# Performance work log

Hardware: AMD Instinct MI355X
Metric: run time of the kernel (lower is better)

## Reference

```python
import jax, jax.numpy as jnp
import numpy as np

EMBED_DIM = 1024
HEAD_NUM = 16
NEG = 100000.0


def setup_inputs() -> dict:
    key = jax.random.key(0)
    k1, k2, k3, k4, k5 = jax.random.split(key, 5)
    B, S, E = 2, 2048, EMBED_DIM
    return {
        "x": jax.random.normal(k1, (B, S, E), dtype=jnp.float32),
        "w_attn": jax.random.normal(k2, (E, 3 * E), dtype=jnp.float32) * 0.02,
        "b_attn": jax.random.normal(k3, (3 * E,), dtype=jnp.float32) * 0.02,
        "w_proj": jax.random.normal(k4, (E, E), dtype=jnp.float32) * 0.02,
        "b_proj": jax.random.normal(k5, (E,), dtype=jnp.float32) * 0.02,
    }


def reference(x, w_attn, b_attn, w_proj, b_proj):
    B, S, E = x.shape
    H = HEAD_NUM
    d = E // H
    dk = jnp.asarray(d, x.dtype) ** 0.5  # (embed_dim // head_num) ** 0.5

    qkv = x @ w_attn + b_attn                      # [B, S, 3E]
    qkv = qkv.reshape(B, S, H, 3 * d)              # split heads BEFORE chunk (as in source)
    qkv = jnp.swapaxes(qkv, 1, 2)                  # [B, H, S, 3d]
    q, k, v = jnp.split(qkv, 3, axis=-1)           # each [B, H, S, d]

    w = jnp.einsum("bhqd,bhkd->bhqk", q, k) / dk   # [B, H, S, S]
    mask = jnp.tril(jnp.ones((S, S), dtype=x.dtype))
    w = w * mask - (1.0 - mask) * NEG              # exact masking math of source
    w = jax.nn.softmax(w, axis=-1)                 # dropout omitted (eval mode)

    a = jnp.einsum("bhqk,bhkd->bhqd", w, v)        # [B, H, S, d]
    a = jnp.swapaxes(a, 1, 2).reshape(B, S, E)     # [B, S, E]
    h = a @ w_proj + b_proj                        # resi dropout omitted (eval mode)
    return h
```

## Files before the change

### kernel.cpp

```cpp
#include <hip/hip_runtime.h>
#include <hip/hip_bf16.h>

#define BB 2
#define SS 2048
#define EE 1024
#define HH 16
#define DD 64
#define MM (BB*SS)
#define N1 (3*EE)

typedef __attribute__((ext_vector_type(4))) float f32x4;
typedef __attribute__((ext_vector_type(16))) float f32x16;
typedef __attribute__((ext_vector_type(8))) short bf16x8;
typedef __attribute__((ext_vector_type(4))) unsigned int u32x4;
typedef __attribute__((ext_vector_type(2))) unsigned int u32x2;

__device__ __forceinline__ ushort f2bf(float f){
  union { float f; unsigned u; } v; v.f = f;
  unsigned r = v.u + 0x7fffu + ((v.u >> 16) & 1u);
  return (ushort)(r >> 16);
}

__device__ __forceinline__ float bf2f(ushort u){
  union { unsigned u; float f; } v; v.u = ((unsigned)u) << 16; return v.f;
}

__device__ __forceinline__ unsigned cvt_pk(float a, float b){
  unsigned r; asm("v_cvt_pk_bf16_f32 %0, %1, %2" : "=v"(r) : "v"(a), "v"(b)); return r;
}

__device__ __forceinline__ float exp2_fast(float x){
  float r; asm("v_exp_f32 %0, %1" : "=v"(r) : "v"(x)); return r;
}

__device__ __forceinline__ u32x2 pl32swap(unsigned a, unsigned b){
  return __builtin_amdgcn_permlane32_swap(a, b, false, false);
}

__device__ __forceinline__ void gload16(const void* g, void* l){
  __builtin_amdgcn_global_load_lds(
      (const __attribute__((address_space(1))) unsigned*)g,
      (__attribute__((address_space(3))) unsigned*)l, 16, 0, 0);
}

__global__ __launch_bounds__(256) void prep_kernel(const float* __restrict__ x, ushort* __restrict__ xb,
    const float* __restrict__ wa, ushort* __restrict__ waT,
    const float* __restrict__ wp, ushort* __restrict__ wpT){
  __shared__ float t[32][33];
  const int bid = blockIdx.x, tid = threadIdx.x;
  if (bid < 4096){
    int i = bid*256 + tid;
    const float4 f = reinterpret_cast<const float4*>(x)[i];
    ushort4 o; o.x=f2bf(f.x); o.y=f2bf(f.y); o.z=f2bf(f.z); o.w=f2bf(f.w);
    reinterpret_cast<ushort4*>(xb)[i] = o;
  } else {
    const float* in; ushort* out; int N, nx, b;
    if (bid < 7168){ b = bid - 4096; in = wa; out = waT; N = N1; nx = N1/32; }
    else           { b = bid - 7168; in = wp; out = wpT; N = EE; nx = EE/32; }
    const int n0 = (b % nx)*32, k0 = (b / nx)*32;
    const int tx = tid & 31, ty = tid >> 5;
    for (int r = ty; r < 32; r += 8)
      t[r][tx] = in[(size_t)(k0+r)*N + n0 + tx];
    __syncthreads();
    for (int r = ty; r < 32; r += 8)
      out[(size_t)(n0+r)*EE + k0 + tx] = f2bf(t[tx][r]);
  }
}

__global__ __launch_bounds__(256) void gemm_qkv(const ushort* __restrict__ A,
    const ushort* __restrict__ Bt, const float* __restrict__ bias,
    ushort* __restrict__ q_, ushort* __restrict__ k_, ushort* __restrict__ v_,
    int M, int N, int K){
  __shared__ ushort As[128*64];
  __shared__ ushort Bs[128*64];
  const int tid = threadIdx.x;
  const int lane = tid & 63, w = tid >> 6;
  const int nx = gridDim.x;
  const int nwg = nx * gridDim.y;
  const int flat = blockIdx.y*nx + blockIdx.x;
  const int sw = (flat & 7)*(nwg >> 3) + (flat >> 3);
  const int m0 = (sw / nx)*128, n0 = (sw % nx)*128;
  const int wm = (w >> 1)*64, wn = (w & 1)*64;
  const int lr = lane & 15, g4 = lane >> 4;
  const int c0 = w*4;
  const int csr = lane >> 3;
  const int gcb = ((lane & 7) ^ csr)*8;
  const int sw7 = lr & 7;

  f32x4 acc[4][4] = {};
  for (int k0 = 0; k0 < K; k0 += 64){
    #pragma unroll
    for (int i = 0; i < 4; ++i){
      const int c = c0 + i;
      gload16(A  + (size_t)(m0 + c*8 + csr)*K + k0 + gcb, &As[(c*8)*64]);
      gload16(Bt + (size_t)(n0 + c*8 + csr)*K + k0 + gcb, &Bs[(c*8)*64]);
    }
    __syncthreads();
    #pragma unroll
    for (int kk = 0; kk < 2; ++kk){
      bf16x8 af[4], bfr[4];
      #pragma unroll
      for (int m = 0; m < 4; ++m)
        af[m] = *reinterpret_cast<bf16x8*>(&As[(wm + m*16 + lr)*64 + (((kk*4 + g4) ^ sw7)*8)]);
      #pragma unroll
      for (int n = 0; n < 4; ++n)
        bfr[n] = *reinterpret_cast<bf16x8*>(&Bs[(wn + n*16 + lr)*64 + (((kk*4 + g4) ^ sw7)*8)]);
      __builtin_amdgcn_s_setprio(1);
      #pragma unroll
      for (int m = 0; m < 4; ++m)
        #pragma unroll
        for (int n = 0; n < 4; ++n)
          acc[m][n] = __builtin_amdgcn_mfma_f32_16x16x32_bf16(af[m], bfr[n], acc[m][n], 0, 0, 0);
      __builtin_amdgcn_s_setprio(0);
    }
    __syncthreads();
  }
  #pragma unroll
  for (int m = 0; m < 4; ++m){
    #pragma unroll
    for (int n = 0; n < 4; ++n){
      int col = n0 + wn + n*16 + lr;
      float bv = bias[col];
      #pragma unroll
      for (int r = 0; r < 4; ++r){
        int row = m0 + wm + m*16 + (lane >> 4)*4 + r;
        float v = acc[m][n][r] + bv;
        int b = row >> 11, s = row & 2047;
        int h = col / 192, t = col - h*192;
        ushort u = f2bf(v);
        size_t bh = (size_t)(b*HH + h);
        if (t < 64)       q_[(bh*SS + s)*DD + t]        = u;
        else if (t < 128) k_[(bh*SS + s)*DD + (t-64)]   = u;
        else              v_[(bh*DD + (t-128))*SS + s]  = u;
      }
    }
  }
}

__global__ __launch_bounds__(256) void gemm_proj(const ushort* __restrict__ A,
    const ushort* __restrict__ Bt, const float* __restrict__ bias,
    float* __restrict__ of, int M, int N, int K){
  __shared__ ushort As[64*64];
  __shared__ ushort Bs[128*64];
  const int tid = threadIdx.x;
  const int lane = tid & 63, w = tid >> 6;
  const int nx = gridDim.x;
  const int nwg = nx * gridDim.y;
  const int flat = blockIdx.y*nx + blockIdx.x;
  const int sw = (flat & 7)*(nwg >> 3) + (flat >> 3);
  const int m0 = (sw / nx)*64, n0 = (sw % nx)*128;
  const int lr = lane & 15, g4 = lane >> 4;
  const int csr = lane >> 3;
  const int gcb = ((lane & 7) ^ csr)*8;
  const int sw7 = lr & 7;

  f32x4 acc[4][2] = {};
  for (int k0 = 0; k0 < K; k0 += 64){
    #pragma unroll
    for (int i = 0; i < 2; ++i){
      const int c = w*2 + i;
      gload16(A + (size_t)(m0 + c*8 + csr)*K + k0 + gcb, &As[(c*8)*64]);
    }
    #pragma unroll
    for (int i = 0; i < 4; ++i){
      const int c = w*4 + i;
      gload16(Bt + (size_t)(n0 + c*8 + csr)*K + k0 + gcb, &Bs[(c*8)*64]);
    }
    __syncthreads();
    #pragma unroll
    for (int kk = 0; kk < 2; ++kk){
      bf16x8 af[4], bfr[2];
      #pragma unroll
      for (int m = 0; m < 4; ++m)
        af[m] = *reinterpret_cast<bf16x8*>(&As[(m*16 + lr)*64 + (((kk*4 + g4) ^ sw7)*8)]);
      #pragma unroll
      for (int n = 0; n < 2; ++n)
        bfr[n] = *reinterpret_cast<bf16x8*>(&Bs[(w*32 + n*16 + lr)*64 + (((kk*4 + g4) ^ sw7)*8)]);
      __builtin_amdgcn_s_setprio(1);
      #pragma unroll
      for (int m = 0; m < 4; ++m)
        #pragma unroll
        for (int n = 0; n < 2; ++n)
          acc[m][n] = __builtin_amdgcn_mfma_f32_16x16x32_bf16(af[m], bfr[n], acc[m][n], 0, 0, 0);
      __builtin_amdgcn_s_setprio(0);
    }
    __syncthreads();
  }
  #pragma unroll
  for (int m = 0; m < 4; ++m){
    #pragma unroll
    for (int n = 0; n < 2; ++n){
      int col = n0 + w*32 + n*16 + lr;
      float bv = bias[col];
      #pragma unroll
      for (int r = 0; r < 4; ++r){
        int row = m0 + m*16 + g4*4 + r;
        of[(size_t)row*N + col] = acc[m][n][r] + bv;
      }
    }
  }
}

#define SCL 0.18033688f
__global__ __launch_bounds__(256,3) void attn2(const ushort* __restrict__ Qg,
    const ushort* __restrict__ Kg, const ushort* __restrict__ Vg,
    ushort* __restrict__ aout, ushort* __restrict__ pbuf,
    float* __restrict__ s0b, float* __restrict__ s1b){
  __shared__ __align__(16) ushort Kl[3][64*64];
  __shared__ __align__(16) ushort Vl[3][64*64];
  const int tid = threadIdx.x, lane = tid & 63, wv = tid >> 6;
  const int bh = blockIdx.x;
  const int c  = blockIdx.y;
  int qt, t0, t1, half;
  if (c < 8){ qt = c; t0 = 0; t1 = 2*(c+1); half = -1; }
  else { int i = c - 8; qt = 8 + (i >> 1); int n = qt + 1; half = i & 1;
         t0 = half ? n : 0; t1 = half ? 2*n : n; }
  const int b = bh >> 4, h = bh & 15;
  const int q0 = qt*128;
  const int ql = lane & 31, g = lane >> 5;
  const int qrow = q0 + wv*32 + ql;
  const int qminw = q0 + wv*32;
  const int qmaxw = qminw + 31;

  const ushort* Qp = Qg + ((size_t)bh*SS + qrow)*DD;
  bf16x8 qf[4];
  #pragma unroll
  for (int s = 0; s < 4; ++s)
    qf[s] = *(const bf16x8*)(Qp + s*16 + g*8);

  f32x16 ot[2] = {};
  float sr = 0.f;

  const int csr = lane >> 3;
  const int gcb = ((lane & 7) ^ csr)*8;
  const ushort* Kbase = Kg + (size_t)bh*SS*DD;
  const ushort* Vbase = Vg + (size_t)bh*DD*SS;
  const int nv = (qmaxw >> 6) + 1;
  const int swq = (ql & 7);

  auto stage = [&](int t, int bi){
    const int k0 = t*64;
    #pragma unroll
    for (int i = 0; i < 2; ++i){
      const int ch = wv*2 + i;
      gload16(Kbase + (size_t)(k0 + ch*8 + csr)*DD + gcb, &Kl[bi][(ch*8)*64]);
      gload16(Vbase + (size_t)(ch*8 + csr)*SS + k0 + gcb, &Vl[bi][(ch*8)*64]);
    }
  };

  auto qk = [&](int t, int bi, f32x16& s0, f32x16& s1){
    const ushort* Kc = &Kl[bi][0];
    f32x16 a0 = {}, a1 = {};
    __builtin_amdgcn_s_setprio(1);
    #pragma unroll
    for (int s = 0; s < 4; ++s){
      bf16x8 kf0 = *(const bf16x8*)&Kc[ ql     *64 + (((2*s + g) ^ swq)*8)];
      bf16x8 kf1 = *(const bf16x8*)&Kc[(32+ql) *64 + (((2*s + g) ^ swq)*8)];
      a0 = __builtin_amdgcn_mfma_f32_32x32x16_bf16(kf0, qf[s], a0, 0, 0, 0);
      a1 = __builtin_amdgcn_mfma_f32_32x32x16_bf16(kf1, qf[s], a1, 0, 0, 0);
    }
    __builtin_amdgcn_s_setprio(0);
    const int k0 = t*64;
    if (k0 + 63 > qminw){
      #pragma unroll
      for (int r = 0; r < 16; ++r){
        int kg0 = k0 + (r & 3) + 8*(r >> 2) + 4*g;
        a0[r] = (kg0 > qrow) ? -1e30f : a0[r];
        a1[r] = (kg0 + 32 > qrow) ? -1e30f : a1[r];
      }
    }
    s0 = a0; s1 = a1;
  };

  auto smpv = [&](int bi, f32x16& s0, f32x16& s1){
    float p[2][16];
    #pragma unroll
    for (int r = 0; r < 16; ++r){
      p[0][r] = exp2_fast(s0[r]*SCL);
      p[1][r] = exp2_fast(s1[r]*SCL);
    }
    float s8[8];
    #pragma unroll
    for (int i = 0; i < 8; ++i)
      s8[i] = (p[0][i] + p[0][i+8]) + (p[1][i] + p[1][i+8]);
    float ts = ((s8[0]+s8[1]) + (s8[2]+s8[3])) + ((s8[4]+s8[5]) + (s8[6]+s8[7]));
    { u32x2 rs = pl32swap(__float_as_uint(ts), __float_as_uint(ts));
      ts = __uint_as_float(rs[0]) + __uint_as_float(rs[1]); }
    sr += ts;

    const ushort* Vc = &Vl[bi][0];
    __builtin_amdgcn_s_setprio(1);
    #pragma unroll
    for (int kf = 0; kf < 2; ++kf){
      #pragma unroll
      for (int s2 = 0; s2 < 2; ++s2){
        const int base = s2*8;
        unsigned u0 = cvt_pk(p[kf][base+0], p[kf][base+1]);
        unsigned u1 = cvt_pk(p[kf][base+2], p[kf][base+3]);
        unsigned u2 = cvt_pk(p[kf][base+4], p[kf][base+5]);
        unsigned u3 = cvt_pk(p[kf][base+6], p[kf][base+7]);
        u32x2 r0 = pl32swap(u0, u2);
        u32x2 r1 = pl32swap(u1, u3);
        union { u32x4 u; bf16x8 hv; } pw;
        pw.u[0] = r0[0]; pw.u[1] = r1[0]; pw.u[2] = r0[1]; pw.u[3] = r1[1];
        const int cbv = 4*kf + 2*s2 + g;
        bf16x8 v0f = *(const bf16x8*)&Vc[ ql     *64 + ((cbv ^ swq)*8)];
        bf16x8 v1f = *(const bf16x8*)&Vc[(32+ql) *64 + ((cbv ^ swq)*8)];
        ot[0] = __builtin_amdgcn_mfma_f32_32x32x16_bf16(v0f, pw.hv, ot[0], 0, 0, 0);
        ot[1] = __builtin_amdgcn_mfma_f32_32x32x16_bf16(v1f, pw.hv, ot[1], 0, 0, 0);
      }
    }
    __builtin_amdgcn_s_setprio(0);
  };

  stage(t0, 0);
  stage(t0 + 1, 1);
  int bi = 0;
  for (int t = t0; t < t1; ++t){
    if (t + 1 < t1) { asm volatile("s_waitcnt vmcnt(4)" ::: "memory"); }
    else            { asm volatile("s_waitcnt vmcnt(0)" ::: "memory"); }
    __builtin_amdgcn_s_barrier();
    __builtin_amdgcn_sched_barrier(0);
    if (t + 2 < t1){
      int bs = bi + 2; if (bs >= 3) bs -= 3;
      stage(t + 2, bs);
    }
    if (t < nv){
      f32x16 s0, s1;
      qk(t, bi, s0, s1);
      smpv(bi, s0, s1);
    }
    ++bi; if (bi == 3) bi = 0;
  }

  const float inv = 1.f / sr;
  if (half == 1){
    const int pr = ((qt - 8)*32 + bh)*128 + wv*32 + ql;
    #pragma unroll
    for (int df = 0; df < 2; ++df){
      #pragma unroll
      for (int t = 0; t < 4; ++t){
        ushort4 o4;
        o4.x = f2bf(ot[df][t*4+0]*inv);
        o4.y = f2bf(ot[df][t*4+1]*inv);
        o4.z = f2bf(ot[df][t*4+2]*inv);
        o4.w = f2bf(ot[df][t*4+3]*inv);
        int d = df*32 + 8*t + 4*g;
        *(ushort4*)&pbuf[(size_t)pr*64 + d] = o4;
      }
    }
    if (g == 0) s1b[pr] = sr;
  } else {
    const size_t obase = ((size_t)b*SS + qrow)*EE + h*DD;
    #pragma unroll
    for (int df = 0; df < 2; ++df){
      #pragma unroll
      for (int t = 0; t < 4; ++t){
        ushort4 o4;
        o4.x = f2bf(ot[df][t*4+0]*inv);
        o4.y = f2bf(ot[df][t*4+1]*inv);
        o4.z = f2bf(ot[df][t*4+2]*inv);
        o4.w = f2bf(ot[df][t*4+3]*inv);
        int d = df*32 + 8*t + 4*g;
        *(ushort4*)&aout[obase + d] = o4;
      }
    }
    if (half == 0){
      const int pr = ((qt - 8)*32 + bh)*128 + wv*32 + ql;
      if (g == 0) s0b[pr] = sr;
    }
  }
}

__global__ __launch_bounds__(256) void combine_kernel(ushort* __restrict__ ab,
    const ushort* __restrict__ pbuf, const float* __restrict__ s0b,
    const float* __restrict__ s1b){
  const int idx = blockIdx.x*256 + threadIdx.x;
  const int d4 = (idx & 15)*4;
  const int rr = (idx >> 4) & 127;
  const int pb = idx >> 11;
  const int qt8 = pb >> 5, bh = pb & 31;
  const int b = bh >> 4, h = bh & 15;
  const int pr = pb*128 + rr;
  const float s0 = s0b[pr], s1 = s1b[pr];
  const float wn = 1.f/(s0 + s1);
  const float w0 = s0*wn, w1 = s1*wn;
  const size_t ao = ((size_t)(b*SS + (8 + qt8)*128 + rr))*EE + h*DD + d4;
  const size_t po = (size_t)pr*64 + d4;
  ushort4 a = *(const ushort4*)&ab[ao];
  ushort4 p = *(const ushort4*)&pbuf[po];
  ushort4 o;
  o.x = f2bf(w0*bf2f(a.x) + w1*bf2f(p.x));
  o.y = f2bf(w0*bf2f(a.y) + w1*bf2f(p.y));
  o.z = f2bf(w0*bf2f(a.z) + w1*bf2f(p.z));
  o.w = f2bf(w0*bf2f(a.w) + w1*bf2f(p.w));
  *(ushort4*)&ab[ao] = o;
}

extern "C" void kernel_launch(void* const* d_in, const int* in_sizes, int n_in,
                              void* d_out, int out_size, void* d_ws, size_t ws_size,
                              hipStream_t stream){
  const float* x      = (const float*)d_in[0];
  const float* w_attn = (const float*)d_in[1];
  const float* b_attn = (const float*)d_in[2];
  const float* w_proj = (const float*)d_in[3];
  const float* b_proj = (const float*)d_in[4];
  float* out = (float*)d_out;

  ushort* ws   = (ushort*)d_ws;
  ushort* xb   = ws;
  ushort* waT  = xb  + (size_t)MM*EE;
  ushort* wpT  = waT + (size_t)N1*EE;
  ushort* qb_  = wpT + (size_t)EE*EE;
  ushort* kb_  = qb_ + (size_t)MM*EE;
  ushort* vTb  = kb_ + (size_t)MM*EE;
  ushort* ab   = vTb + (size_t)MM*EE;
  ushort* pbuf = xb;
  float*  s0b  = (float*)waT;
  float*  s1b  = s0b + 8*32*128;

  prep_kernel<<<8192, 256, 0, stream>>>(x, xb, w_attn, waT, w_proj, wpT);
  gemm_qkv<<<dim3(N1/128, MM/128), 256, 0, stream>>>(xb, waT, b_attn, qb_, kb_, vTb, MM, N1, EE);
  attn2<<<dim3(BB*HH, 24), 256, 0, stream>>>(qb_, kb_, vTb, ab, pbuf, s0b, s1b);
  combine_kernel<<<2048, 256, 0, stream>>>(ab, pbuf, s0b, s1b);
  gemm_proj<<<dim3(EE/128, MM/64), 256, 0, stream>>>(ab, wpT, b_proj, out, MM, EE, EE);
}
```

Baseline: 107.7 us.

## Triple-buffer QKV GEMM shared-memory tiles with async prefetch two steps ahead

The QKV projection GEMM now uses three shared-memory stages with a K-step of 32 instead of a single 64-wide buffer. Global-to-LDS loads for step t+2 are issued before computing step t, and explicit vmcnt waits replace the two per-iteration __syncthreads. The goal is to overlap global memory latency with MFMA work. In exchange there are more loop iterations with less compute each, a new swizzle pattern, and a dependence on hand-counted vmcnt values being correct.

```diff
diff --git a/kernel.cpp b/kernel.cpp
--- a/kernel.cpp
+++ b/kernel.cpp
@@ -71,8 +71,8 @@
     const ushort* __restrict__ Bt, const float* __restrict__ bias,
     ushort* __restrict__ q_, ushort* __restrict__ k_, ushort* __restrict__ v_,
     int M, int N, int K){
-  __shared__ ushort As[128*64];
-  __shared__ ushort Bs[128*64];
+  __shared__ ushort As[3][128*32];
+  __shared__ ushort Bs[3][128*32];
   const int tid = threadIdx.x;
   const int lane = tid & 63, w = tid >> 6;
   const int nx = gridDim.x;
@@ -82,38 +82,49 @@
   const int m0 = (sw / nx)*128, n0 = (sw % nx)*128;
   const int wm = (w >> 1)*64, wn = (w & 1)*64;
   const int lr = lane & 15, g4 = lane >> 4;
-  const int c0 = w*4;
-  const int csr = lane >> 3;
-  const int gcb = ((lane & 7) ^ csr)*8;
-  const int sw7 = lr & 7;
+  const int srow16 = lane >> 2;
+  const int gsc = ((lane & 3) ^ ((lane >> 3) & 3))*8;
+  const int rsw = (lr >> 1) & 3;
+  const int NT = K >> 5;
+
+  auto stage = [&](int t, int bi){
+    const int k0 = t*32;
+    #pragma unroll
+    for (int i = 0; i < 2; ++i){
+      const int c = w*2 + i;
+      gload16(A  + (size_t)(m0 + c*16 + srow16)*K + k0 + gsc, &As[bi][(c*16)*32]);
+      gload16(Bt + (size_t)(n0 + c*16 + srow16)*K + k0 + gsc, &Bs[bi][(c*16)*32]);
+    }
+  };
 
   f32x4 acc[4][4] = {};
-  for (int k0 = 0; k0 < K; k0 += 64){
-    #pragma unroll
-    for (int i = 0; i < 4; ++i){
-      const int c = c0 + i;
-      gload16(A  + (size_t)(m0 + c*8 + csr)*K + k0 + gcb, &As[(c*8)*64]);
-      gload16(Bt + (size_t)(n0 + c*8 + csr)*K + k0 + gcb, &Bs[(c*8)*64]);
-    }
-    __syncthreads();
-    #pragma unroll
-    for (int kk = 0; kk < 2; ++kk){
-      bf16x8 af[4], bfr[4];
-      #pragma unroll
-      for (int m = 0; m < 4; ++m)
-        af[m] = *reinterpret_cast<bf16x8*>(&As[(wm + m*16 + lr)*64 + (((kk*4 + g4) ^ sw7)*8)]);
+  stage(0, 0);
+  stage(1, 1);
+  int bi = 0;
+  for (int t = 0; t < NT; ++t){
+    if (t + 1 < NT) { asm volatile("s_waitcnt vmcnt(4)" ::: "memory"); }
+    else            { asm volatile("s_waitcnt vmcnt(0)" ::: "memory"); }
+    __builtin_amdgcn_s_barrier();
+    __builtin_amdgcn_sched_barrier(0);
+    if (t + 2 < NT){
+      int bs = bi + 2; if (bs >= 3) bs -= 3;
+      stage(t + 2, bs);
+    }
+    bf16x8 af[4], bfr[4];
+    #pragma unroll
+    for (int m = 0; m < 4; ++m)
+      af[m] = *reinterpret_cast<bf16x8*>(&As[bi][(wm + m*16 + lr)*32 + ((g4 ^ rsw)*8)]);
+    #pragma unroll
+    for (int n = 0; n < 4; ++n)
+      bfr[n] = *reinterpret_cast<bf16x8*>(&Bs[bi][(wn + n*16 + lr)*32 + ((g4 ^ rsw)*8)]);
+    __builtin_amdgcn_s_setprio(1);
+    #pragma unroll
+    for (int m = 0; m < 4; ++m)
       #pragma unroll
       for (int n = 0; n < 4; ++n)
-        bfr[n] = *reinterpret_cast<bf16x8*>(&Bs[(wn + n*16 + lr)*64 + (((kk*4 + g4) ^ sw7)*8)]);
-      __builtin_amdgcn_s_setprio(1);
-      #pragma unroll
-      for (int m = 0; m < 4; ++m)
-        #pragma unroll
-        for (int n = 0; n < 4; ++n)
-          acc[m][n] = __builtin_amdgcn_mfma_f32_16x16x32_bf16(af[m], bfr[n], acc[m][n], 0, 0, 0);
-      __builtin_amdgcn_s_setprio(0);
-    }
-    __syncthreads();
+        acc[m][n] = __builtin_amdgcn_mfma_f32_16x16x32_bf16(af[m], bfr[n], acc[m][n], 0, 0, 0);
+    __builtin_amdgcn_s_setprio(0);
+    ++bi; if (bi == 3) bi = 0;
   }
   #pragma unroll
   for (int m = 0; m < 4; ++m){
```

Result: slower. 110.9 us (+3.0%).
